# Performance work log

Measured on AMD Instinct MI355X. Metric: run time of the kernel, lower is better.

Reference implementation:

```python
import jax, jax.numpy as jnp
import numpy as np

EMBED_DIM = 1024
NUM_HEADS = 16
HEAD_DIM = EMBED_DIM // NUM_HEADS
SCALE = HEAD_DIM ** -0.5


def setup_inputs() -> dict:
    key = jax.random.key(0)
    ks = jax.random.split(key, 9)
    B, N = 2, 2048
    s = EMBED_DIM ** -0.5  # ~ torch Linear init scale
    x = jax.random.normal(ks[0], (B, N, EMBED_DIM), dtype=jnp.float32)
    Wq = jax.random.uniform(ks[1], (EMBED_DIM, EMBED_DIM), jnp.float32, -s, s)
    bq = jax.random.uniform(ks[2], (EMBED_DIM,), jnp.float32, -s, s)
    Wk = jax.random.uniform(ks[3], (EMBED_DIM, EMBED_DIM), jnp.float32, -s, s)
    bk = jax.random.uniform(ks[4], (EMBED_DIM,), jnp.float32, -s, s)
    Wv = jax.random.uniform(ks[5], (EMBED_DIM, EMBED_DIM), jnp.float32, -s, s)
    bv = jax.random.uniform(ks[6], (EMBED_DIM,), jnp.float32, -s, s)
    Wo = jax.random.uniform(ks[7], (EMBED_DIM, EMBED_DIM), jnp.float32, -s, s)
    bo = jax.random.uniform(ks[8], (EMBED_DIM,), jnp.float32, -s, s)
    return {"x": x, "Wq": Wq, "bq": bq, "Wk": Wk, "bk": bk,
            "Wv": Wv, "bv": bv, "Wo": Wo, "bo": bo}


def reference(x, Wq, bq, Wk, bk, Wv, bv, Wo, bo):
    B, N, R = x.shape
    H, D = NUM_HEADS, HEAD_DIM
    # projections: Linear(x) = x @ W^T + b; reshape to (B, H, N, D)
    def proj(W, b):
        return (x @ W.T + b).reshape(B, N, H, D).transpose(0, 2, 1, 3)
    q = proj(Wq, bq)
    k = proj(Wk, bk)
    v = proj(Wv, bv)
    attn = jnp.einsum('bhnd,bhmd->bhnm', q, k) * SCALE  # (B,H,N,N)
    attn = jax.nn.softmax(attn, axis=-1)
    out = jnp.einsum('bhnm,bhmd->bhnd', attn, v)        # (B,H,N,D)
    out = out.transpose(0, 2, 1, 3).reshape(B, N, R)
    return out @ Wo.T + bo
```

## Files before the change

### kernel.cpp

```cpp
#include <hip/hip_runtime.h>
#include <stdint.h>

typedef __bf16 bf16;
typedef __bf16 bf16x4 __attribute__((ext_vector_type(4)));
typedef __bf16 bf16x8 __attribute__((ext_vector_type(8)));
typedef float f32x4 __attribute__((ext_vector_type(4)));
typedef short short4_t __attribute__((ext_vector_type(4)));

#define MFMA16(a, b, c) __builtin_amdgcn_mfma_f32_16x16x32_bf16((a), (b), (c), 0, 0, 0)

__device__ __forceinline__ f32x4 mfma1k(bf16x4 a, bf16x4 b, f32x4 c) {
    return __builtin_amdgcn_mfma_f32_16x16x16bf16_1k(
        __builtin_bit_cast(short4_t, a), __builtin_bit_cast(short4_t, b), c, 0, 0, 0);
}

#define EMBED 1024
#define SEQ   2048
#define MROWS 4096
#define ATTN_SCALE 0.125f

__device__ __forceinline__ void gl2lds16(const bf16* g, bf16* l) {
    __builtin_amdgcn_global_load_lds(
        (const __attribute__((address_space(1))) void*)g,
        (__attribute__((address_space(3))) void*)l,
        16, 0, 0);
}

__global__ __launch_bounds__(256) void cast_all_kernel(
    const float* __restrict__ x,  const float* __restrict__ Wq,
    const float* __restrict__ Wk, const float* __restrict__ Wv,
    const float* __restrict__ Wo, bf16* __restrict__ dst) {
    const int blk = blockIdx.x;
    const float* src;
    size_t so, dofs;
    if (blk < 2048) {
        src = x; so = (size_t)blk * 2048; dofs = so;
    } else {
        const int w = (blk - 2048) >> 9;
        so  = (size_t)((blk - 2048) & 511) * 2048;
        src = (w == 0) ? Wq : (w == 1) ? Wk : (w == 2) ? Wv : Wo;
        dofs = (size_t)(4 + w) * 1024 * 1024 + so;
    }
    const size_t i = (size_t)threadIdx.x * 8;
    float4 a = *(const float4*)(src + so + i);
    float4 b = *(const float4*)(src + so + i + 4);
    bf16x8 o;
    o[0] = (bf16)a.x; o[1] = (bf16)a.y; o[2] = (bf16)a.z; o[3] = (bf16)a.w;
    o[4] = (bf16)b.x; o[5] = (bf16)b.y; o[6] = (bf16)b.z; o[7] = (bf16)b.w;
    *(bf16x8*)(dst + dofs + i) = o;
}

template <bool SCALE>
__device__ __forceinline__ void gemm_tile(const bf16* __restrict__ A,
                                          const bf16* __restrict__ W,
                                          const float* __restrict__ bias,
                                          bf16* __restrict__ C,
                                          int m0, int n0, bf16* smem) {
    bf16* As = smem;
    bf16* Bs = smem + 128 * 64;

    const int lane = threadIdx.x & 63;
    const int wv   = threadIdx.x >> 6;
    const int wm   = (wv >> 1) * 64;
    const int wn   = (wv & 1) * 64;
    const int fr   = lane & 15;
    const int quad = lane >> 4;
    const int srow = wv * 8 + (lane >> 3);
    const int swz  = (((lane & 7) ^ ((lane >> 3) & 7))) * 8;

    f32x4 acc[4][4];
#pragma unroll
    for (int mt = 0; mt < 4; ++mt)
#pragma unroll
        for (int nt = 0; nt < 4; ++nt)
            acc[mt][nt] = (f32x4){0.f, 0.f, 0.f, 0.f};

    for (int k0 = 0; k0 < 1024; k0 += 64) {
#pragma unroll
        for (int i = 0; i < 4; ++i) {
            gl2lds16(A + (size_t)(m0 + i * 32 + srow) * 1024 + k0 + swz,
                     &As[(i * 32 + wv * 8) * 64]);
            gl2lds16(W + (size_t)(n0 + i * 32 + srow) * 1024 + k0 + swz,
                     &Bs[(i * 32 + wv * 8) * 64]);
        }
        __syncthreads();
#pragma unroll
        for (int ks = 0; ks < 2; ++ks) {
            const int fcol = ((ks * 4 + quad) ^ (fr & 7)) * 8;
            bf16x8 af[4], bfr[4];
#pragma unroll
            for (int t = 0; t < 4; ++t) {
                af[t]  = *(const bf16x8*)&As[(wm + t * 16 + fr) * 64 + fcol];
                bfr[t] = *(const bf16x8*)&Bs[(wn + t * 16 + fr) * 64 + fcol];
            }
#pragma unroll
            for (int mt = 0; mt < 4; ++mt)
#pragma unroll
                for (int nt = 0; nt < 4; ++nt)
                    acc[mt][nt] = MFMA16(af[mt], bfr[nt], acc[mt][nt]);
        }
        __syncthreads();
    }

    float bv[4];
#pragma unroll
    for (int nt = 0; nt < 4; ++nt)
        bv[nt] = bias[n0 + wn + nt * 16 + fr];
    const int row4 = quad * 4;
#pragma unroll
    for (int mt = 0; mt < 4; ++mt)
#pragma unroll
        for (int nt = 0; nt < 4; ++nt)
#pragma unroll
            for (int r = 0; r < 4; ++r) {
                int m = m0 + wm + mt * 16 + row4 + r;
                int n = n0 + wn + nt * 16 + fr;
                float v = acc[mt][nt][r] + bv[nt];
                if (SCALE) v *= ATTN_SCALE;
                C[(size_t)m * 1024 + n] = (bf16)v;
            }
}

__device__ __forceinline__ void v_tile(const bf16* __restrict__ x,
                                       const bf16* __restrict__ Wv,
                                       const float* __restrict__ bias,
                                       bf16* __restrict__ VT,
                                       int m0, int n0, bf16* smem) {
    bf16* As = smem;
    bf16* Bs = smem + 128 * 64;

    const int lane = threadIdx.x & 63;
    const int wv   = threadIdx.x >> 6;
    const int wmW  = (wv >> 1) * 64;
    const int wnT  = (wv & 1) * 64;
    const int f    = lane & 15;
    const int quad = lane >> 4;
    const int srow = wv * 8 + (lane >> 3);
    const int swz  = (((lane & 7) ^ ((lane >> 3) & 7))) * 8;

    f32x4 acc[4][4];
#pragma unroll
    for (int mt = 0; mt < 4; ++mt)
#pragma unroll
        for (int nt = 0; nt < 4; ++nt)
            acc[mt][nt] = (f32x4){0.f, 0.f, 0.f, 0.f};

    for (int k0 = 0; k0 < 1024; k0 += 64) {
#pragma unroll
        for (int i = 0; i < 4; ++i) {
            gl2lds16(x  + (size_t)(m0 + i * 32 + srow) * 1024 + k0 + swz,
                     &As[(i * 32 + wv * 8) * 64]);
            gl2lds16(Wv + (size_t)(n0 + i * 32 + srow) * 1024 + k0 + swz,
                     &Bs[(i * 32 + wv * 8) * 64]);
        }
        __syncthreads();
#pragma unroll
        for (int ks = 0; ks < 2; ++ks) {
            const int fcol = ((ks * 4 + quad) ^ (f & 7)) * 8;
            bf16x8 wf[4], xf[4];
#pragma unroll
            for (int t = 0; t < 4; ++t) {
                wf[t] = *(const bf16x8*)&Bs[(wmW + t * 16 + f) * 64 + fcol];
                xf[t] = *(const bf16x8*)&As[(wnT + t * 16 + f) * 64 + fcol];
            }
#pragma unroll
            for (int mt = 0; mt < 4; ++mt)
#pragma unroll
                for (int nt = 0; nt < 4; ++nt)
                    acc[mt][nt] = MFMA16(wf[mt], xf[nt], acc[mt][nt]);
        }
        __syncthreads();
    }

    float4 b4[4];
#pragma unroll
    for (int mt = 0; mt < 4; ++mt)
        b4[mt] = *(const float4*)&bias[n0 + wmW + mt * 16 + quad * 4];

#pragma unroll
    for (int mt = 0; mt < 4; ++mt)
#pragma unroll
        for (int nt = 0; nt < 4; ++nt) {
            const int tok = wnT + nt * 16 + f;
#pragma unroll
            for (int r = 0; r < 4; ++r) {
                const float bvr = (r == 0) ? b4[mt].x : (r == 1) ? b4[mt].y
                                : (r == 2) ? b4[mt].z : b4[mt].w;
                smem[(wmW + mt * 16 + quad * 4 + r) * 136 + tok] =
                    (bf16)(acc[mt][nt][r] + bvr);
            }
        }
    __syncthreads();

    const int n_r  = threadIdx.x >> 4;
    const int t8   = (threadIdx.x & 15) * 8;
    const int bb   = m0 >> 11;
    const int tokg = (m0 & 2047) + t8;
#pragma unroll
    for (int p = 0; p < 8; ++p) {
        const int n_loc = p * 16 + n_r;
        bf16x8 v = *(const bf16x8*)&smem[n_loc * 136 + t8];
        *(bf16x8*)&VT[((size_t)(bb * 1024 + n0 + n_loc)) * 2048 + tokg] = v;
    }
}

__global__ __launch_bounds__(256) void qkv_kernel(
    const bf16* __restrict__ x,
    const bf16* __restrict__ Wq, const float* __restrict__ bq,
    const bf16* __restrict__ Wk, const float* __restrict__ bk,
    const bf16* __restrict__ Wv, const float* __restrict__ bv,
    bf16* __restrict__ Q, bf16* __restrict__ K, bf16* __restrict__ VT) {
    __shared__ __align__(16) bf16 smem[128 * 136];
    const int m0    = blockIdx.x * 128;
    const int which = blockIdx.y >> 3;
    const int n0    = (blockIdx.y & 7) * 128;
    if (which == 0)      gemm_tile<true>(x, Wq, bq, Q, m0, n0, smem);
    else if (which == 1) gemm_tile<false>(x, Wk, bk, K, m0, n0, smem);
    else                 v_tile(x, Wv, bv, VT, m0, n0, smem);
}

__global__ __launch_bounds__(256) void oproj_kernel(
    const bf16* __restrict__ A, const bf16* __restrict__ W,
    const float* __restrict__ bias, float* __restrict__ C) {
    const int m0 = blockIdx.x * 128;
    const int n0 = blockIdx.y * 64;

    __shared__ bf16 As[128 * 64];
    __shared__ bf16 Bs[64 * 64];

    const int lane = threadIdx.x & 63;
    const int wv   = threadIdx.x >> 6;
    const int wm   = (wv >> 1) * 64;
    const int wn   = (wv & 1) * 32;
    const int fr   = lane & 15;
    const int quad = lane >> 4;
    const int srow = wv * 8 + (lane >> 3);
    const int swz  = (((lane & 7) ^ ((lane >> 3) & 7))) * 8;

    f32x4 acc[4][2];
#pragma unroll
    for (int mt = 0; mt < 4; ++mt)
#pragma unroll
        for (int nt = 0; nt < 2; ++nt)
            acc[mt][nt] = (f32x4){0.f, 0.f, 0.f, 0.f};

    for (int k0 = 0; k0 < 1024; k0 += 64) {
#pragma unroll
        for (int i = 0; i < 4; ++i)
            gl2lds16(A + (size_t)(m0 + i * 32 + srow) * 1024 + k0 + swz,
                     &As[(i * 32 + wv * 8) * 64]);
#pragma unroll
        for (int i = 0; i < 2; ++i)
            gl2lds16(W + (size_t)(n0 + i * 32 + srow) * 1024 + k0 + swz,
                     &Bs[(i * 32 + wv * 8) * 64]);
        __syncthreads();
#pragma unroll
        for (int ks = 0; ks < 2; ++ks) {
            const int fcol = ((ks * 4 + quad) ^ (fr & 7)) * 8;
            bf16x8 af[4], bfr[2];
#pragma unroll
            for (int t = 0; t < 4; ++t)
                af[t] = *(const bf16x8*)&As[(wm + t * 16 + fr) * 64 + fcol];
#pragma unroll
            for (int t = 0; t < 2; ++t)
                bfr[t] = *(const bf16x8*)&Bs[(wn + t * 16 + fr) * 64 + fcol];
#pragma unroll
            for (int mt = 0; mt < 4; ++mt)
#pragma unroll
                for (int nt = 0; nt < 2; ++nt)
                    acc[mt][nt] = MFMA16(af[mt], bfr[nt], acc[mt][nt]);
        }
        __syncthreads();
    }

    float bv[2];
#pragma unroll
    for (int nt = 0; nt < 2; ++nt)
        bv[nt] = bias[n0 + wn + nt * 16 + fr];
    const int row4 = quad * 4;
#pragma unroll
    for (int mt = 0; mt < 4; ++mt)
#pragma unroll
        for (int nt = 0; nt < 2; ++nt)
#pragma unroll
            for (int r = 0; r < 4; ++r) {
                int m = m0 + wm + mt * 16 + row4 + r;
                int n = n0 + wn + nt * 16 + fr;
                C[(size_t)m * 1024 + n] = acc[mt][nt][r] + bv[nt];
            }
}

__global__ __launch_bounds__(512) void attn_kernel(
    const bf16* __restrict__ Q, const bf16* __restrict__ K,
    const bf16* __restrict__ VT, bf16* __restrict__ O) {
    const int tid  = threadIdx.x;
    const int lane = tid & 63;
    const int wv   = tid >> 6;
    const int quad = lane >> 4;
    const int f    = lane & 15;
    const int q0   = blockIdx.x * 128;
    const int b    = blockIdx.y >> 4;
    const int h    = blockIdx.y & 15;

    const bf16* Qp = Q + ((size_t)b * SEQ) * 1024 + (size_t)h * 64;
    const bf16* Kp = K + ((size_t)b * SEQ) * 1024 + (size_t)h * 64;
    const bf16* Vp = VT + ((size_t)(b * 1024 + h * 64)) * 2048;
    bf16*       Op = O + ((size_t)b * SEQ) * 1024 + (size_t)h * 64;

    __shared__ bf16 Ks[2][64 * 64];
    __shared__ bf16 VTs[2][64 * 64];

    bf16x8 qf[2];
    {
        const bf16* qrow = Qp + (size_t)(q0 + wv * 16 + f) * 1024;
        qf[0] = *(const bf16x8*)(qrow + quad * 8);
        qf[1] = *(const bf16x8*)(qrow + 32 + quad * 8);
    }

    const int srow = tid >> 3;
    const int swz  = (((tid & 7) ^ ((tid >> 3) & 7))) * 8;
    auto stageK = [&](int kv0, int buf) {
        gl2lds16(Kp + (size_t)(kv0 + srow) * 1024 + swz, &Ks[buf][wv * 512]);
    };
    auto stageVT = [&](int kv0, int buf) {
        gl2lds16(Vp + (size_t)srow * 2048 + kv0 + swz, &VTs[buf][wv * 512]);
    };

    stageK(0, 0);
    stageVT(0, 0);

    f32x4 oacc[4];
#pragma unroll
    for (int t = 0; t < 4; ++t)
        oacc[t] = (f32x4){0.f, 0.f, 0.f, 0.f};
    f32x4 lacc = (f32x4){0.f, 0.f, 0.f, 0.f};
    const bf16x4 onesb = {(bf16)1.f, (bf16)1.f, (bf16)1.f, (bf16)1.f};
    const f32x4  zero4 = (f32x4){0.f, 0.f, 0.f, 0.f};

    const int fcol0 = (quad ^ (f & 7)) * 8;
    const int fcol1 = ((4 + quad) ^ (f & 7)) * 8;

    __syncthreads();

    auto step = [&](int cur, int nextit) {
        if (nextit < SEQ / 64) {
            stageK(nextit * 64, cur ^ 1);
            stageVT(nextit * 64, cur ^ 1);
        }

        f32x4 s[4];
#pragma unroll
        for (int t = 0; t < 4; ++t) {
            bf16x8 k0 = *(const bf16x8*)&Ks[cur][(t * 16 + f) * 64 + fcol0];
            bf16x8 k1 = *(const bf16x8*)&Ks[cur][(t * 16 + f) * 64 + fcol1];
            s[t] = MFMA16(k0, qf[0], zero4);
            s[t] = MFMA16(k1, qf[1], s[t]);
        }

        bf16x4 pb[4];
#pragma unroll
        for (int t = 0; t < 4; ++t) {
#pragma unroll
            for (int r = 0; r < 4; ++r)
                pb[t][r] = (bf16)__expf(s[t][r]);
            lacc = mfma1k(onesb, pb[t], lacc);
        }

#pragma unroll
        for (int dt = 0; dt < 4; ++dt) {
#pragma unroll
            for (int kt = 0; kt < 4; ++kt) {
                const int pc = ((kt * 2 + (quad >> 1)) ^ (f & 7)) * 8 + (quad & 1) * 4;
                bf16x4 vf = *(const bf16x4*)&VTs[cur][(dt * 16 + f) * 64 + pc];
                oacc[dt] = mfma1k(vf, pb[kt], oacc[dt]);
            }
        }
        __syncthreads();
    };

    for (int it = 0; it < SEQ / 64; it += 2) {
        step(0, it + 1);
        step(1, it + 2);
    }

    const float inv = 1.0f / lacc[0];
    bf16* orow = Op + (size_t)(q0 + wv * 16 + f) * 1024;
#pragma unroll
    for (int dt = 0; dt < 4; ++dt) {
        bf16x4 ov;
#pragma unroll
        for (int r = 0; r < 4; ++r)
            ov[r] = (bf16)(oacc[dt][r] * inv);
        *(bf16x4*)(orow + dt * 16 + quad * 4) = ov;
    }
}

extern "C" void kernel_launch(void* const* d_in, const int* in_sizes, int n_in,
                              void* d_out, int out_size, void* d_ws, size_t ws_size,
                              hipStream_t stream) {
    const float* x  = (const float*)d_in[0];
    const float* Wq = (const float*)d_in[1];
    const float* bq = (const float*)d_in[2];
    const float* Wk = (const float*)d_in[3];
    const float* bk = (const float*)d_in[4];
    const float* Wv = (const float*)d_in[5];
    const float* bv = (const float*)d_in[6];
    const float* Wo = (const float*)d_in[7];
    const float* bo = (const float*)d_in[8];
    float* out = (float*)d_out;

    bf16* xb  = (bf16*)d_ws;
    bf16* Wqb = xb  + (size_t)MROWS * 1024;
    bf16* Wkb = Wqb + (size_t)1024 * 1024;
    bf16* Wvb = Wkb + (size_t)1024 * 1024;
    bf16* Wob = Wvb + (size_t)1024 * 1024;
    bf16* Q   = Wob + (size_t)1024 * 1024;
    bf16* K   = Q + (size_t)MROWS * 1024;
    bf16* VT  = K + (size_t)MROWS * 1024;
    bf16* O   = VT + (size_t)MROWS * 1024;

    cast_all_kernel<<<4096, 256, 0, stream>>>(x, Wq, Wk, Wv, Wo, xb);

    qkv_kernel<<<dim3(32, 24), 256, 0, stream>>>(xb, Wqb, bq, Wkb, bk, Wvb, bv, Q, K, VT);
    attn_kernel<<<dim3(16, 32), 512, 0, stream>>>(Q, K, VT, O);
    oproj_kernel<<<dim3(32, 16), 256, 0, stream>>>(O, Wob, bo, out);
}
```

Before: 201.5 us.

## Split attention KV range across two blocks and register-block four query groups per wave

The attention kernel now uses 256-thread blocks where each wave handles 64 query rows (four 16-row groups). K fragments loaded from LDS are reused across all four groups, and each V fragment feeds four MFMAs. The KV sequence is split into two halves processed by separate blocks. Each block writes an unnormalized partial output and a row sum, and a new combine kernel adds the halves and normalizes. This cuts LDS traffic per MFMA and keeps the block count unchanged, at the cost of more registers, an extra kernel launch and extra global traffic for the partials.

```diff
diff --git a/kernel.cpp b/kernel.cpp
--- a/kernel.cpp
+++ b/kernel.cpp
@@ -290,50 +290,68 @@
             }
 }
 
-__global__ __launch_bounds__(512) void attn_kernel(
+__global__ __launch_bounds__(256, 2) void attn_kernel(
     const bf16* __restrict__ Q, const bf16* __restrict__ K,
-    const bf16* __restrict__ VT, bf16* __restrict__ O) {
+    const bf16* __restrict__ VT, bf16* __restrict__ Opart,
+    float* __restrict__ lpart) {
     const int tid  = threadIdx.x;
     const int lane = tid & 63;
     const int wv   = tid >> 6;
     const int quad = lane >> 4;
     const int f    = lane & 15;
-    const int q0   = blockIdx.x * 128;
+    const int qt   = blockIdx.x >> 1;
+    const int half = blockIdx.x & 1;
+    const int q0   = qt * 256;
+    const int kvb  = half * 1024;
     const int b    = blockIdx.y >> 4;
     const int h    = blockIdx.y & 15;
 
     const bf16* Qp = Q + ((size_t)b * SEQ) * 1024 + (size_t)h * 64;
     const bf16* Kp = K + ((size_t)b * SEQ) * 1024 + (size_t)h * 64;
     const bf16* Vp = VT + ((size_t)(b * 1024 + h * 64)) * 2048;
-    bf16*       Op = O + ((size_t)b * SEQ) * 1024 + (size_t)h * 64;
+    bf16*  Op = Opart + (size_t)half * MROWS * 1024
+                      + ((size_t)b * SEQ) * 1024 + (size_t)h * 64;
+    float* lp = lpart + ((size_t)(half * 2 + b) * 16 + h) * SEQ;
 
     __shared__ bf16 Ks[2][64 * 64];
     __shared__ bf16 VTs[2][64 * 64];
 
-    bf16x8 qf[2];
-    {
-        const bf16* qrow = Qp + (size_t)(q0 + wv * 16 + f) * 1024;
-        qf[0] = *(const bf16x8*)(qrow + quad * 8);
-        qf[1] = *(const bf16x8*)(qrow + 32 + quad * 8);
-    }
-
-    const int srow = tid >> 3;
-    const int swz  = (((tid & 7) ^ ((tid >> 3) & 7))) * 8;
+    bf16x8 qf[4][2];
+#pragma unroll
+    for (int qg = 0; qg < 4; ++qg) {
+        const bf16* qrow = Qp + (size_t)(q0 + wv * 64 + qg * 16 + f) * 1024;
+        qf[qg][0] = *(const bf16x8*)(qrow + quad * 8);
+        qf[qg][1] = *(const bf16x8*)(qrow + 32 + quad * 8);
+    }
+
+    const int srow = wv * 8 + (lane >> 3);
+    const int swz  = (((lane & 7) ^ ((lane >> 3) & 7))) * 8;
     auto stageK = [&](int kv0, int buf) {
-        gl2lds16(Kp + (size_t)(kv0 + srow) * 1024 + swz, &Ks[buf][wv * 512]);
+#pragma unroll
+        for (int i = 0; i < 2; ++i)
+            gl2lds16(Kp + (size_t)(kv0 + i * 32 + srow) * 1024 + swz,
+                     &Ks[buf][(i * 32 + wv * 8) * 64]);
     };
     auto stageVT = [&](int kv0, int buf) {
-        gl2lds16(Vp + (size_t)srow * 2048 + kv0 + swz, &VTs[buf][wv * 512]);
+#pragma unroll
+        for (int i = 0; i < 2; ++i)
+            gl2lds16(Vp + (size_t)(i * 32 + srow) * 2048 + kv0 + swz,
+                     &VTs[buf][(i * 32 + wv * 8) * 64]);
     };
 
-    stageK(0, 0);
-    stageVT(0, 0);
-
-    f32x4 oacc[4];
-#pragma unroll
-    for (int t = 0; t < 4; ++t)
-        oacc[t] = (f32x4){0.f, 0.f, 0.f, 0.f};
-    f32x4 lacc = (f32x4){0.f, 0.f, 0.f, 0.f};
+    stageK(kvb, 0);
+    stageVT(kvb, 0);
+
+    f32x4 oacc[4][4];
+#pragma unroll
+    for (int qg = 0; qg < 4; ++qg)
+#pragma unroll
+        for (int t = 0; t < 4; ++t)
+            oacc[qg][t] = (f32x4){0.f, 0.f, 0.f, 0.f};
+    f32x4 lacc[4];
+#pragma unroll
+    for (int qg = 0; qg < 4; ++qg)
+        lacc[qg] = (f32x4){0.f, 0.f, 0.f, 0.f};
     const bf16x4 onesb = {(bf16)1.f, (bf16)1.f, (bf16)1.f, (bf16)1.f};
     const f32x4  zero4 = (f32x4){0.f, 0.f, 0.f, 0.f};
 
@@ -343,27 +361,33 @@
     __syncthreads();
 
     auto step = [&](int cur, int nextit) {
-        if (nextit < SEQ / 64) {
-            stageK(nextit * 64, cur ^ 1);
-            stageVT(nextit * 64, cur ^ 1);
-        }
-
-        f32x4 s[4];
+        if (nextit < 16) {
+            stageK(kvb + nextit * 64, cur ^ 1);
+            stageVT(kvb + nextit * 64, cur ^ 1);
+        }
+
+        bf16x8 kf0[4], kf1[4];
 #pragma unroll
         for (int t = 0; t < 4; ++t) {
-            bf16x8 k0 = *(const bf16x8*)&Ks[cur][(t * 16 + f) * 64 + fcol0];
-            bf16x8 k1 = *(const bf16x8*)&Ks[cur][(t * 16 + f) * 64 + fcol1];
-            s[t] = MFMA16(k0, qf[0], zero4);
-            s[t] = MFMA16(k1, qf[1], s[t]);
-        }
-
-        bf16x4 pb[4];
-#pragma unroll
-        for (int t = 0; t < 4; ++t) {
-#pragma unroll
-            for (int r = 0; r < 4; ++r)
-                pb[t][r] = (bf16)__expf(s[t][r]);
-            lacc = mfma1k(onesb, pb[t], lacc);
+            kf0[t] = *(const bf16x8*)&Ks[cur][(t * 16 + f) * 64 + fcol0];
+            kf1[t] = *(const bf16x8*)&Ks[cur][(t * 16 + f) * 64 + fcol1];
+        }
+        bf16x4 pb[4][4];
+#pragma unroll
+        for (int qg = 0; qg < 4; ++qg) {
+            f32x4 s[4];
+#pragma unroll
+            for (int t = 0; t < 4; ++t) {
+                s[t] = MFMA16(kf0[t], qf[qg][0], zero4);
+                s[t] = MFMA16(kf1[t], qf[qg][1], s[t]);
+            }
+#pragma unroll
+            for (int t = 0; t < 4; ++t) {
+#pragma unroll
+                for (int r = 0; r < 4; ++r)
+                    pb[qg][t][r] = (bf16)__expf(s[t][r]);
+                lacc[qg] = mfma1k(onesb, pb[qg][t], lacc[qg]);
+            }
         }
 
 #pragma unroll
@@ -372,27 +396,58 @@
             for (int kt = 0; kt < 4; ++kt) {
                 const int pc = ((kt * 2 + (quad >> 1)) ^ (f & 7)) * 8 + (quad & 1) * 4;
                 bf16x4 vf = *(const bf16x4*)&VTs[cur][(dt * 16 + f) * 64 + pc];
-                oacc[dt] = mfma1k(vf, pb[kt], oacc[dt]);
+#pragma unroll
+                for (int qg = 0; qg < 4; ++qg)
+                    oacc[qg][dt] = mfma1k(vf, pb[qg][kt], oacc[qg][dt]);
             }
         }
         __syncthreads();
     };
 
-    for (int it = 0; it < SEQ / 64; it += 2) {
+    for (int it = 0; it < 16; it += 2) {
         step(0, it + 1);
         step(1, it + 2);
     }
 
-    const float inv = 1.0f / lacc[0];
-    bf16* orow = Op + (size_t)(q0 + wv * 16 + f) * 1024;
-#pragma unroll
-    for (int dt = 0; dt < 4; ++dt) {
-        bf16x4 ov;
-#pragma unroll
-        for (int r = 0; r < 4; ++r)
-            ov[r] = (bf16)(oacc[dt][r] * inv);
-        *(bf16x4*)(orow + dt * 16 + quad * 4) = ov;
-    }
+#pragma unroll
+    for (int qg = 0; qg < 4; ++qg) {
+        const int q = q0 + wv * 64 + qg * 16 + f;
+        bf16* orow = Op + (size_t)q * 1024;
+#pragma unroll
+        for (int dt = 0; dt < 4; ++dt) {
+            bf16x4 ov;
+#pragma unroll
+            for (int r = 0; r < 4; ++r)
+                ov[r] = (bf16)oacc[qg][dt][r];
+            *(bf16x4*)(orow + dt * 16 + quad * 4) = ov;
+        }
+        if (quad == 0)
+            lp[q] = lacc[qg][0];
+    }
+}
+
+__global__ __launch_bounds__(256) void combine_kernel(
+    const bf16* __restrict__ Opart, const float* __restrict__ lpart,
+    bf16* __restrict__ O) {
+    const int gid = blockIdx.x * 256 + threadIdx.x;
+    const int row = gid >> 7;
+    const int c8  = (gid & 127) * 8;
+    const int b   = row >> 11;
+    const int tok = row & 2047;
+    const int h   = c8 >> 6;
+
+    const float l = lpart[((size_t)(0 * 2 + b) * 16 + h) * SEQ + tok]
+                  + lpart[((size_t)(1 * 2 + b) * 16 + h) * SEQ + tok];
+    const float inv = 1.0f / l;
+
+    const size_t off = (size_t)row * 1024 + c8;
+    bf16x8 a = *(const bf16x8*)&Opart[off];
+    bf16x8 c = *(const bf16x8*)&Opart[(size_t)MROWS * 1024 + off];
+    bf16x8 o;
+#pragma unroll
+    for (int i = 0; i < 8; ++i)
+        o[i] = (bf16)(((float)a[i] + (float)c[i]) * inv);
+    *(bf16x8*)&O[off] = o;
 }
 
 extern "C" void kernel_launch(void* const* d_in, const int* in_sizes, int n_in,
@@ -409,19 +464,22 @@
     const float* bo = (const float*)d_in[8];
     float* out = (float*)d_out;
 
-    bf16* xb  = (bf16*)d_ws;
-    bf16* Wqb = xb  + (size_t)MROWS * 1024;
-    bf16* Wkb = Wqb + (size_t)1024 * 1024;
-    bf16* Wvb = Wkb + (size_t)1024 * 1024;
-    bf16* Wob = Wvb + (size_t)1024 * 1024;
-    bf16* Q   = Wob + (size_t)1024 * 1024;
-    bf16* K   = Q + (size_t)MROWS * 1024;
-    bf16* VT  = K + (size_t)MROWS * 1024;
-    bf16* O   = VT + (size_t)MROWS * 1024;
+    bf16* xb    = (bf16*)d_ws;
+    bf16* Wqb   = xb   + (size_t)MROWS * 1024;
+    bf16* Wkb   = Wqb  + (size_t)1024 * 1024;
+    bf16* Wvb   = Wkb  + (size_t)1024 * 1024;
+    bf16* Wob   = Wvb  + (size_t)1024 * 1024;
+    bf16* Q     = Wob  + (size_t)1024 * 1024;
+    bf16* K     = Q    + (size_t)MROWS * 1024;
+    bf16* VT    = K    + (size_t)MROWS * 1024;
+    bf16* O     = VT   + (size_t)MROWS * 1024;
+    bf16* Opart = O    + (size_t)MROWS * 1024;
+    float* lpart = (float*)(Opart + (size_t)2 * MROWS * 1024);
 
     cast_all_kernel<<<4096, 256, 0, stream>>>(x, Wq, Wk, Wv, Wo, xb);
 
     qkv_kernel<<<dim3(32, 24), 256, 0, stream>>>(xb, Wqb, bq, Wkb, bk, Wvb, bv, Q, K, VT);
-    attn_kernel<<<dim3(16, 32), 512, 0, stream>>>(Q, K, VT, O);
+    attn_kernel<<<dim3(16, 32), 256, 0, stream>>>(Q, K, VT, Opart, lpart);
+    combine_kernel<<<2048, 256, 0, stream>>>(Opart, lpart, O);
     oproj_kernel<<<dim3(32, 16), 256, 0, stream>>>(O, Wob, bo, out);
 }
```

After: 200.8 us. Within noise of the previous version (-0.3%).
